# Kernel optimization log

Hardware: AMD Instinct MI355X
Metric: run time of the kernel (lower is better)

Reference implementation:

```python
import jax, jax.numpy as jnp
import numpy as np

B, T, C = 4, 2048, 1024
NH = 16
HS = C // NH


def setup_inputs() -> dict:
    key = jax.random.key(0)
    ks = jax.random.split(key, 11)
    s = 1.0 / np.sqrt(C)
    inp = {
        "query": jax.random.normal(ks[0], (B, T, C), jnp.float32),
        "key": jax.random.normal(ks[1], (B, T, C), jnp.float32),
        "value": jax.random.normal(ks[2], (B, T, C), jnp.float32),
        # causal mask: 1.0 where attention is disallowed (j > i)
        "mask": jnp.triu(jnp.ones((T, T), jnp.float32), k=1)[None, None, :, :],
        "Wq": jax.random.normal(ks[3], (C, C), jnp.float32) * s,
        "bq": jnp.zeros((C,), jnp.float32),
        "Wk": jax.random.normal(ks[4], (C, C), jnp.float32) * s,
        "bk": jnp.zeros((C,), jnp.float32),
        "Wv": jax.random.normal(ks[5], (C, C), jnp.float32) * s,
        "bv": jnp.zeros((C,), jnp.float32),
        "Wo": jax.random.normal(ks[6], (C, C), jnp.float32) * s,
        "bo": jnp.zeros((C,), jnp.float32),
    }
    return inp


def _split_heads(x):  # [B,T,C] -> [B,NH,T,HS]
    Bq, Tq, Cq = x.shape
    return x.reshape(Bq, Tq, NH, Cq // NH).transpose(0, 2, 1, 3)


def reference(query, key, value, mask, Wq, bq, Wk, bk, Wv, bv, Wo, bo):
    q = _split_heads(query @ Wq + bq)   # [B,NH,T,HS]
    k = _split_heads(key @ Wk + bk)
    v = _split_heads(value @ Wv + bv)
    scores = jnp.einsum("bhqd,bhkd->bhqk", q, k) / jnp.sqrt(jnp.asarray(HS, q.dtype))
    scores = scores + mask * (-1e9)
    attn = jax.nn.softmax(scores, axis=-1)
    out = jnp.einsum("bhqk,bhkd->bhqd", attn, v)     # [B,NH,T,HS]
    out = out.transpose(0, 2, 1, 3).reshape(query.shape[0], query.shape[1], -1)
    return out @ Wo + bo
```

## Files before the change

kernel.cpp:

```cpp
#include <hip/hip_runtime.h>
#include <hip/hip_bf16.h>
#include <stdint.h>

#define B_ 4
#define T_ 2048
#define C_ 1024
#define NH_ 16
#define HS_ 64

using bf16 = __hip_bfloat16;
typedef __bf16 bf16x8 __attribute__((ext_vector_type(8)));
typedef float f32x4 __attribute__((ext_vector_type(4)));
typedef short short8 __attribute__((ext_vector_type(8)));

__device__ __forceinline__ f32x4 mfma16(bf16x8 a, bf16x8 b, f32x4 c) {
    return __builtin_amdgcn_mfma_f32_16x16x32_bf16(a, b, c, 0, 0, 0);
}

__device__ __forceinline__ float fexp2(float x) {
    return __builtin_amdgcn_exp2f(x);
}

__device__ __forceinline__ short bf16bits(float f) {
    __bf16 b = (__bf16)f;
    return *reinterpret_cast<short*>(&b);
}

__device__ __forceinline__ void gload16(const void* g, void* l) {
    __builtin_amdgcn_global_load_lds(
        (const __attribute__((address_space(1))) void*)g,
        (__attribute__((address_space(3))) void*)l, 16, 0, 0);
}

__device__ __forceinline__ short8 load8(const bf16* p) { return *(const short8*)p; }
__device__ __forceinline__ short8 load8(const float* p) {
    float4 f0 = *(const float4*)p;
    float4 f1 = *(const float4*)(p + 4);
    short8 r;
    r[0] = bf16bits(f0.x); r[1] = bf16bits(f0.y); r[2] = bf16bits(f0.z); r[3] = bf16bits(f0.w);
    r[4] = bf16bits(f1.x); r[5] = bf16bits(f1.y); r[6] = bf16bits(f1.z); r[7] = bf16bits(f1.w);
    return r;
}

__device__ __forceinline__ void storev(bf16* p, float v) { *p = __float2bfloat16(v); }
__device__ __forceinline__ void storev(float* p, float v) { *p = v; }

__device__ __forceinline__ int swz64(int row, int bytecol) {
    return row * 64 + ((((bytecol >> 4) ^ row) & 3) << 4) + (bytecol & 15);
}

template <typename InT>
__device__ __forceinline__ void transpose_body(
    const InT* __restrict__ in, bf16* __restrict__ out, int R, int C, int zb)
{
    __shared__ short tile[64][80];
    const int t = threadIdx.x;
    const size_t batch = (size_t)zb * R * C;
    const int bx = blockIdx.x * 64;
    const int by = blockIdx.y * 64;
    const int r = t >> 3, c8 = (t & 7) * 8;

    *(short8*)&tile[r][c8]      = load8(in + batch + (size_t)(by + r) * C + bx + c8);
    *(short8*)&tile[r + 32][c8] = load8(in + batch + (size_t)(by + r + 32) * C + bx + c8);
    __syncthreads();
    short8 v0, v1;
    #pragma unroll
    for (int i = 0; i < 8; ++i) {
        v0[i] = tile[c8 + i][r];
        v1[i] = tile[c8 + i][r + 32];
    }
    *(short8*)(out + batch + (size_t)(bx + r) * R + by + c8)      = v0;
    *(short8*)(out + batch + (size_t)(bx + r + 32) * R + by + c8) = v1;
}

__global__ __launch_bounds__(256) void transpose_v_kernel(
    const bf16* __restrict__ in, bf16* __restrict__ out)
{
    transpose_body<bf16>(in, out, T_, HS_, blockIdx.z);
}

__global__ __launch_bounds__(256) void transpose_w4_kernel(
    const float* __restrict__ Wq, const float* __restrict__ Wk,
    const float* __restrict__ Wv, const float* __restrict__ Wo,
    bf16* __restrict__ WqT, bf16* __restrict__ WkT,
    bf16* __restrict__ WvT, bf16* __restrict__ WoT)
{
    const int z = blockIdx.z;
    const float* in = (z == 0) ? Wq : (z == 1) ? Wk : (z == 2) ? Wv : Wo;
    bf16* out      = (z == 0) ? WqT : (z == 1) ? WkT : (z == 2) ? WvT : WoT;
    transpose_body<float>(in, out, 1024, 1024, 0);
}

template <int MODE, typename AT, typename OutT>
__device__ __forceinline__ void gemm_body(
    const AT* __restrict__ A, const bf16* __restrict__ BT,
    const float* __restrict__ bias, OutT* __restrict__ out,
    int M, int N, int K)
{
    constexpr bool A_BF16 = (sizeof(AT) == 2);
    __shared__ __align__(16) short As[128 * 32];
    __shared__ __align__(16) short Bs[128 * 32];
    const int tid = threadIdx.x;
    const int lane = tid & 63;
    const int w = tid >> 6;
    const int wm = w >> 1, wn = w & 1;
    const int lg = lane >> 4, lr = lane & 15;
    const int bm = blockIdx.x * 128;
    const int bn = blockIdx.y * 128;

    const int grow = w * 16 + (lane >> 2);
    const int gch  = (lane & 3) ^ (grow & 3);
    const bf16* gB0 = BT + (size_t)(bn + grow) * K + gch * 8;
    const AT*   gA0 = A  + (size_t)(bm + grow) * K + gch * 8;
    char* lB0 = (char*)Bs + w * 1024;
    char* lA0 = (char*)As + w * 1024;

    const int sr = tid >> 2;
    const int sc = (tid & 3) * 16;
    const AT* gA = A + (size_t)(bm + sr) * K + (tid & 3) * 8;

    f32x4 acc[4][4] = {};

    for (int k0 = 0; k0 < K; k0 += 32) {
        __syncthreads();
        gload16(gB0 + k0, lB0);
        gload16(gB0 + (size_t)64 * K + k0, lB0 + 4096);
        if constexpr (A_BF16) {
            gload16(gA0 + k0, lA0);
            gload16(gA0 + (size_t)64 * K + k0, lA0 + 4096);
        } else {
            short8 a0 = load8(gA + k0);
            short8 a1 = load8(gA + (size_t)64 * K + k0);
            *(short8*)((char*)As + swz64(sr, sc))      = a0;
            *(short8*)((char*)As + swz64(sr + 64, sc)) = a1;
        }
        __syncthreads();
        bf16x8 af[4], bfv[4];
        #pragma unroll
        for (int i = 0; i < 4; ++i) {
            af[i]  = *(const bf16x8*)((char*)As + swz64(wm * 64 + i * 16 + lr, lg * 16));
            bfv[i] = *(const bf16x8*)((char*)Bs + swz64(wn * 64 + i * 16 + lr, lg * 16));
        }
        #pragma unroll
        for (int mi = 0; mi < 4; ++mi)
            #pragma unroll
            for (int nj = 0; nj < 4; ++nj)
                acc[mi][nj] = mfma16(af[mi], bfv[nj], acc[mi][nj]);
    }

    #pragma unroll
    for (int mi = 0; mi < 4; ++mi) {
        #pragma unroll
        for (int nj = 0; nj < 4; ++nj) {
            const int n = bn + wn * 64 + nj * 16 + lr;
            const float bv = bias[n];
            #pragma unroll
            for (int r = 0; r < 4; ++r) {
                const int m = bm + wm * 64 + mi * 16 + lg * 4 + r;
                const float val = acc[mi][nj][r] + bv;
                size_t idx;
                if (MODE == 1) {
                    idx = (size_t)((m >> 11) * NH_ + (n >> 6)) * (T_ * HS_)
                        + (size_t)(m & (T_ - 1)) * HS_ + (n & (HS_ - 1));
                } else {
                    idx = (size_t)m * N + n;
                }
                storev(out + idx, val);
            }
        }
    }
}

__global__ __launch_bounds__(256) void gemm_qkv_kernel(
    const float* __restrict__ Xq, const float* __restrict__ Xk, const float* __restrict__ Xv,
    const bf16* __restrict__ WqT, const bf16* __restrict__ WkT, const bf16* __restrict__ WvT,
    const float* __restrict__ bq, const float* __restrict__ bk, const float* __restrict__ bv,
    bf16* __restrict__ Qh, bf16* __restrict__ Kh, bf16* __restrict__ Vh)
{
    const int z = blockIdx.z;
    const float* A  = (z == 0) ? Xq : (z == 1) ? Xk : Xv;
    const bf16* BT  = (z == 0) ? WqT : (z == 1) ? WkT : WvT;
    const float* bs = (z == 0) ? bq : (z == 1) ? bk : bv;
    bf16* out       = (z == 0) ? Qh : (z == 1) ? Kh : Vh;
    gemm_body<1, float, bf16>(A, BT, bs, out, 8192, 1024, 1024);
}

__global__ __launch_bounds__(256) void gemm_out_kernel(
    const bf16* __restrict__ A, const bf16* __restrict__ BT,
    const float* __restrict__ bias, float* __restrict__ out)
{
    gemm_body<0, bf16, float>(A, BT, bias, out, 8192, 1024, 1024);
}

__global__ __launch_bounds__(512, 4) void attn_kernel(
    const bf16* __restrict__ Qh, const bf16* __restrict__ Kh,
    const bf16* __restrict__ Vt, bf16* __restrict__ Ob)
{
    __shared__ __align__(16) char Ks[2][8192];
    __shared__ __align__(16) char Vs[2][8192];
    __shared__ __align__(16) char Ps[8][2][2048];

    const int tid  = threadIdx.x;
    const int lane = tid & 63;
    const int w    = tid >> 6;
    const int lg = lane >> 4, lr = lane & 15;
    const int bh = blockIdx.x;
    const int bq = blockIdx.y;
    const size_t hb = (size_t)bh * (T_ * HS_);

    const int s_lo = bq * 8 + w;
    const int s_hi = 127 - s_lo;
    const int qbase[2] = { s_lo * 16, s_hi * 16 };
    const int last_t[2] = { s_lo >> 2, s_hi >> 2 };
    const int nt = 32 - 2 * bq;

    const int swzp = (lr & 7) << 4;
    const float SC = 0.125f * 1.44269504088896f;

    const int strow = tid >> 3;
    const int stch  = tid & 7;
    const int stdst = strow * 128 + ((stch ^ (strow & 7)) << 4);
    const bf16* gK = Kh + hb + (size_t)strow * HS_ + stch * 8;
    const bf16* gV = Vt + hb + (size_t)strow * T_  + stch * 8;

    bf16x8 qf[2][2];
    #pragma unroll
    for (int qs = 0; qs < 2; ++qs)
        #pragma unroll
        for (int kfi = 0; kfi < 2; ++kfi)
            qf[qs][kfi] = *(const bf16x8*)(Qh + hb + (size_t)(qbase[qs] + lr) * HS_ + kfi * 32 + lg * 8);

    f32x4 accO[2][4] = {};
    float m_s[2] = {-1e30f, -1e30f};
    float l_s[2] = {0.f, 0.f};
    char* pwq[2] = {&Ps[w][0][0], &Ps[w][1][0]};

    uint4 kst = *(const uint4*)(gK);
    uint4 vst = *(const uint4*)(gV);
    *(uint4*)(&Ks[0][stdst]) = kst;
    *(uint4*)(&Vs[0][stdst]) = vst;
    __syncthreads();

    int c = 0;
    for (int t = 0; t < nt; ++t) {
        if (t + 1 < nt) {
            kst = *(const uint4*)(gK + (size_t)(t + 1) * 64 * HS_);
            vst = *(const uint4*)(gV + (t + 1) * 64);
        }
        const int j0 = t * 64;
        const char* Kc = &Ks[c][0];
        const char* Vc = &Vs[c][0];
        const bool act[2] = { t <= last_t[0], t <= last_t[1] };

        bf16x8 kfr[4][2];
        #pragma unroll
        for (int s = 0; s < 4; ++s)
            #pragma unroll
            for (int kfi = 0; kfi < 2; ++kfi)
                kfr[s][kfi] = *(const bf16x8*)(Kc + (s * 16 + lr) * 128 + (((kfi * 4 + lg) ^ (lr & 7)) << 4));

        #pragma unroll
        for (int qs = 0; qs < 2; ++qs) {
            if (!act[qs]) continue;
            f32x4 st[4];
            #pragma unroll
            for (int s = 0; s < 4; ++s) {
                f32x4 a = {};
                #pragma unroll
                for (int kfi = 0; kfi < 2; ++kfi)
                    a = mfma16(kfr[s][kfi], qf[qs][kfi], a);
                st[s] = a;
            }
            float p[4][4];
            #pragma unroll
            for (int s = 0; s < 4; ++s)
                #pragma unroll
                for (int r = 0; r < 4; ++r)
                    p[s][r] = st[s][r] * SC;
            if (t == last_t[qs]) {
                const int q = qbase[qs] + lr;
                #pragma unroll
                for (int s = 0; s < 4; ++s)
                    #pragma unroll
                    for (int r = 0; r < 4; ++r)
                        if (j0 + s * 16 + 4 * lg + r > q) p[s][r] = -1e30f;
            }
            float mx0 = fmaxf(fmaxf(p[0][0], p[0][1]), fmaxf(p[0][2], p[0][3]));
            float mx1 = fmaxf(fmaxf(p[1][0], p[1][1]), fmaxf(p[1][2], p[1][3]));
            float mx2 = fmaxf(fmaxf(p[2][0], p[2][1]), fmaxf(p[2][2], p[2][3]));
            float mx3 = fmaxf(fmaxf(p[3][0], p[3][1]), fmaxf(p[3][2], p[3][3]));
            float mxin = fmaxf(fmaxf(mx0, mx1), fmaxf(mx2, mx3));
            if (!__all(mxin <= m_s[qs] + 8.0f)) {
                float mx = mxin;
                mx = fmaxf(mx, __shfl_xor(mx, 16));
                mx = fmaxf(mx, __shfl_xor(mx, 32));
                const float mnew = fmaxf(m_s[qs], mx);
                const float sf = fexp2(m_s[qs] - mnew);
                m_s[qs] = mnew;
                l_s[qs] *= sf;
                f32x4 sfv;
                #pragma unroll
                for (int r = 0; r < 4; ++r)
                    sfv[r] = __shfl(sf, 4 * lg + r);
                #pragma unroll
                for (int d = 0; d < 4; ++d)
                    accO[qs][d] *= sfv;
            }
            float rs = 0.f;
            #pragma unroll
            for (int s = 0; s < 4; ++s)
                #pragma unroll
                for (int r = 0; r < 4; ++r) {
                    p[s][r] = fexp2(p[s][r] - m_s[qs]);
                    rs += p[s][r];
                }
            l_s[qs] += rs;
            #pragma unroll
            for (int s = 0; s < 4; ++s) {
                uint2 pk;
                pk.x = (uint16_t)bf16bits(p[s][0]) | ((uint32_t)(uint16_t)bf16bits(p[s][1]) << 16);
                pk.y = (uint16_t)bf16bits(p[s][2]) | ((uint32_t)(uint16_t)bf16bits(p[s][3]) << 16);
                *(uint2*)(pwq[qs] + ((lr * 128 + s * 32 + lg * 8) ^ swzp)) = pk;
            }
        }
        __builtin_amdgcn_wave_barrier();

        bf16x8 vfr[4][2];
        #pragma unroll
        for (int d = 0; d < 4; ++d)
            #pragma unroll
            for (int kfi = 0; kfi < 2; ++kfi)
                vfr[d][kfi] = *(const bf16x8*)(Vc + (d * 16 + lr) * 128 + (((kfi * 4 + lg) ^ (lr & 7)) << 4));

        #pragma unroll
        for (int qs = 0; qs < 2; ++qs) {
            if (!act[qs]) continue;
            bf16x8 aP[2];
            #pragma unroll
            for (int kfi = 0; kfi < 2; ++kfi)
                aP[kfi] = *(const bf16x8*)(pwq[qs] + ((lr * 128 + kfi * 64 + lg * 16) ^ swzp));
            #pragma unroll
            for (int d = 0; d < 4; ++d)
                #pragma unroll
                for (int kfi = 0; kfi < 2; ++kfi)
                    accO[qs][d] = mfma16(aP[kfi], vfr[d][kfi], accO[qs][d]);
        }

        if (t + 1 < nt) {
            *(uint4*)(&Ks[c ^ 1][stdst]) = kst;
            *(uint4*)(&Vs[c ^ 1][stdst]) = vst;
        }
        __syncthreads();
        c ^= 1;
    }

    const int b = bh >> 4, h = bh & 15;
    #pragma unroll
    for (int qs = 0; qs < 2; ++qs) {
        float lsv[4];
        #pragma unroll
        for (int r = 0; r < 4; ++r) {
            float acc = 0.f;
            #pragma unroll
            for (int g = 0; g < 4; ++g)
                acc += __shfl(l_s[qs], 4 * lg + r + 16 * g);
            lsv[r] = acc;
        }
        #pragma unroll
        for (int d = 0; d < 4; ++d)
            #pragma unroll
            for (int r = 0; r < 4; ++r) {
                const int q = qbase[qs] + 4 * lg + r;
                const float o = accO[qs][d][r] / lsv[r];
                Ob[(((size_t)b * T_ + q) * NH_ + h) * HS_ + d * 16 + lr] = __float2bfloat16(o);
            }
    }
}

extern "C" void kernel_launch(void* const* d_in, const int* in_sizes, int n_in,
                              void* d_out, int out_size, void* d_ws, size_t ws_size,
                              hipStream_t stream)
{
    (void)in_sizes; (void)n_in; (void)out_size; (void)ws_size;
    const float* Xq = (const float*)d_in[0];
    const float* Xk = (const float*)d_in[1];
    const float* Xv = (const float*)d_in[2];
    const float* Wq = (const float*)d_in[4];
    const float* bq = (const float*)d_in[5];
    const float* Wk = (const float*)d_in[6];
    const float* bk = (const float*)d_in[7];
    const float* Wv = (const float*)d_in[8];
    const float* bv = (const float*)d_in[9];
    const float* Wo = (const float*)d_in[10];
    const float* bo = (const float*)d_in[11];

    char* ws = (char*)d_ws;
    bf16* WqT = (bf16*)(ws + ((size_t)0  << 20));
    bf16* WkT = (bf16*)(ws + ((size_t)2  << 20));
    bf16* WvT = (bf16*)(ws + ((size_t)4  << 20));
    bf16* WoT = (bf16*)(ws + ((size_t)6  << 20));
    bf16* Qh  = (bf16*)(ws + ((size_t)8  << 20));
    bf16* Kh  = (bf16*)(ws + ((size_t)24 << 20));
    bf16* Vh  = (bf16*)(ws + ((size_t)40 << 20));
    bf16* VtG = (bf16*)(ws + ((size_t)56 << 20));
    bf16* Ob  = (bf16*)(ws + ((size_t)72 << 20));

    dim3 blk(256);
    transpose_w4_kernel<<<dim3(16, 16, 4), blk, 0, stream>>>(
        Wq, Wk, Wv, Wo, WqT, WkT, WvT, WoT);

    gemm_qkv_kernel<<<dim3(64, 8, 3), blk, 0, stream>>>(
        Xq, Xk, Xv, WqT, WkT, WvT, bq, bk, bv, Qh, Kh, Vh);

    transpose_v_kernel<<<dim3(1, 32, B_ * NH_), blk, 0, stream>>>(Vh, VtG);

    attn_kernel<<<dim3(64, 8), dim3(512), 0, stream>>>(Qh, Kh, VtG, Ob);

    gemm_out_kernel<<<dim3(64, 8), blk, 0, stream>>>(Ob, WoT, bo, (float*)d_out);
}
```

Baseline: 210.1 us.

## Write V transposed from QKV GEMM and double GEMM K-tile to 64

The QKV GEMM epilogue now writes V directly in the per-head transposed layout the attention kernel reads, which removes the separate V transpose kernel, one launch and a round trip of V through memory. Separately, the GEMM K step grows from 32 to 64, using wider LDS tiles with an 8-chunk XOR swizzle, so there are half as many barrier-separated load/compute iterations. The transposed V store is strided along T, so those writes are less coalesced. The larger shared-memory tiles may also reduce occupancy.

```diff
diff --git a/kernel.cpp b/kernel.cpp
--- a/kernel.cpp
+++ b/kernel.cpp
@@ -44,10 +44,6 @@
 
 __device__ __forceinline__ void storev(bf16* p, float v) { *p = __float2bfloat16(v); }
 __device__ __forceinline__ void storev(float* p, float v) { *p = v; }
-
-__device__ __forceinline__ int swz64(int row, int bytecol) {
-    return row * 64 + ((((bytecol >> 4) ^ row) & 3) << 4) + (bytecol & 15);
-}
 
 template <typename InT>
 __device__ __forceinline__ void transpose_body(
@@ -73,12 +69,6 @@
     *(short8*)(out + batch + (size_t)(bx + r + 32) * R + by + c8) = v1;
 }
 
-__global__ __launch_bounds__(256) void transpose_v_kernel(
-    const bf16* __restrict__ in, bf16* __restrict__ out)
-{
-    transpose_body<bf16>(in, out, T_, HS_, blockIdx.z);
-}
-
 __global__ __launch_bounds__(256) void transpose_w4_kernel(
     const float* __restrict__ Wq, const float* __restrict__ Wk,
     const float* __restrict__ Wv, const float* __restrict__ Wo,
@@ -91,15 +81,15 @@
     transpose_body<float>(in, out, 1024, 1024, 0);
 }
 
-template <int MODE, typename AT, typename OutT>
+template <typename AT, typename OutT>
 __device__ __forceinline__ void gemm_body(
     const AT* __restrict__ A, const bf16* __restrict__ BT,
     const float* __restrict__ bias, OutT* __restrict__ out,
-    int M, int N, int K)
+    int M, int N, int K, int mode)
 {
     constexpr bool A_BF16 = (sizeof(AT) == 2);
-    __shared__ __align__(16) short As[128 * 32];
-    __shared__ __align__(16) short Bs[128 * 32];
+    __shared__ __align__(16) short As[128 * 64];
+    __shared__ __align__(16) short Bs[128 * 64];
     const int tid = threadIdx.x;
     const int lane = tid & 63;
     const int w = tid >> 6;
@@ -108,44 +98,51 @@
     const int bm = blockIdx.x * 128;
     const int bn = blockIdx.y * 128;
 
-    const int grow = w * 16 + (lane >> 2);
-    const int gch  = (lane & 3) ^ (grow & 3);
-    const bf16* gB0 = BT + (size_t)(bn + grow) * K + gch * 8;
-    const AT*   gA0 = A  + (size_t)(bm + grow) * K + gch * 8;
-    char* lB0 = (char*)Bs + w * 1024;
-    char* lA0 = (char*)As + w * 1024;
-
-    const int sr = tid >> 2;
-    const int sc = (tid & 3) * 16;
-    const AT* gA = A + (size_t)(bm + sr) * K + (tid & 3) * 8;
+    const int rowi = lane >> 3;
+    const int gch  = (lane & 7) ^ rowi;
+    const bf16* gB0 = BT + (size_t)(bn + w * 32 + rowi) * K + gch * 8;
+    const AT*   gA0 = A  + (size_t)(bm + w * 32 + rowi) * K + gch * 8;
+    char* lB0 = (char*)Bs + w * 4096;
+    char* lA0 = (char*)As + w * 4096;
+
+    const int arow = tid >> 3;
+    const int achk = tid & 7;
+    const AT* gA = A + (size_t)(bm + arow) * K + achk * 8;
+    const int awsw = (achk ^ (arow & 7)) << 4;
 
     f32x4 acc[4][4] = {};
-
-    for (int k0 = 0; k0 < K; k0 += 32) {
+    const int rsw = lr & 7;
+
+    for (int k0 = 0; k0 < K; k0 += 64) {
         __syncthreads();
-        gload16(gB0 + k0, lB0);
-        gload16(gB0 + (size_t)64 * K + k0, lB0 + 4096);
-        if constexpr (A_BF16) {
-            gload16(gA0 + k0, lA0);
-            gload16(gA0 + (size_t)64 * K + k0, lA0 + 4096);
-        } else {
-            short8 a0 = load8(gA + k0);
-            short8 a1 = load8(gA + (size_t)64 * K + k0);
-            *(short8*)((char*)As + swz64(sr, sc))      = a0;
-            *(short8*)((char*)As + swz64(sr + 64, sc)) = a1;
+        #pragma unroll
+        for (int i = 0; i < 4; ++i) {
+            gload16(gB0 + (size_t)i * 8 * K + k0, lB0 + i * 1024);
+            if constexpr (A_BF16)
+                gload16(gA0 + (size_t)i * 8 * K + k0, lA0 + i * 1024);
+        }
+        if constexpr (!A_BF16) {
+            #pragma unroll
+            for (int j = 0; j < 4; ++j) {
+                short8 a0 = load8(gA + (size_t)j * 32 * K + k0);
+                *(short8*)((char*)As + (arow + j * 32) * 128 + awsw) = a0;
+            }
         }
         __syncthreads();
-        bf16x8 af[4], bfv[4];
-        #pragma unroll
-        for (int i = 0; i < 4; ++i) {
-            af[i]  = *(const bf16x8*)((char*)As + swz64(wm * 64 + i * 16 + lr, lg * 16));
-            bfv[i] = *(const bf16x8*)((char*)Bs + swz64(wn * 64 + i * 16 + lr, lg * 16));
-        }
-        #pragma unroll
-        for (int mi = 0; mi < 4; ++mi)
-            #pragma unroll
-            for (int nj = 0; nj < 4; ++nj)
-                acc[mi][nj] = mfma16(af[mi], bfv[nj], acc[mi][nj]);
+        #pragma unroll
+        for (int kfi = 0; kfi < 2; ++kfi) {
+            bf16x8 af[4], bfv[4];
+            #pragma unroll
+            for (int i = 0; i < 4; ++i) {
+                af[i]  = *(const bf16x8*)((char*)As + (wm * 64 + i * 16 + lr) * 128 + (((kfi * 4 + lg) ^ rsw) << 4));
+                bfv[i] = *(const bf16x8*)((char*)Bs + (wn * 64 + i * 16 + lr) * 128 + (((kfi * 4 + lg) ^ rsw) << 4));
+            }
+            #pragma unroll
+            for (int mi = 0; mi < 4; ++mi)
+                #pragma unroll
+                for (int nj = 0; nj < 4; ++nj)
+                    acc[mi][nj] = mfma16(af[mi], bfv[nj], acc[mi][nj]);
+        }
     }
 
     #pragma unroll
@@ -159,9 +156,12 @@
                 const int m = bm + wm * 64 + mi * 16 + lg * 4 + r;
                 const float val = acc[mi][nj][r] + bv;
                 size_t idx;
-                if (MODE == 1) {
+                if (mode == 1) {
                     idx = (size_t)((m >> 11) * NH_ + (n >> 6)) * (T_ * HS_)
                         + (size_t)(m & (T_ - 1)) * HS_ + (n & (HS_ - 1));
+                } else if (mode == 2) {
+                    idx = (size_t)((m >> 11) * NH_ + (n >> 6)) * (T_ * HS_)
+                        + (size_t)(n & (HS_ - 1)) * T_ + (m & (T_ - 1));
                 } else {
                     idx = (size_t)m * N + n;
                 }
@@ -175,21 +175,21 @@
     const float* __restrict__ Xq, const float* __restrict__ Xk, const float* __restrict__ Xv,
     const bf16* __restrict__ WqT, const bf16* __restrict__ WkT, const bf16* __restrict__ WvT,
     const float* __restrict__ bq, const float* __restrict__ bk, const float* __restrict__ bv,
-    bf16* __restrict__ Qh, bf16* __restrict__ Kh, bf16* __restrict__ Vh)
+    bf16* __restrict__ Qh, bf16* __restrict__ Kh, bf16* __restrict__ VtG)
 {
     const int z = blockIdx.z;
     const float* A  = (z == 0) ? Xq : (z == 1) ? Xk : Xv;
     const bf16* BT  = (z == 0) ? WqT : (z == 1) ? WkT : WvT;
     const float* bs = (z == 0) ? bq : (z == 1) ? bk : bv;
-    bf16* out       = (z == 0) ? Qh : (z == 1) ? Kh : Vh;
-    gemm_body<1, float, bf16>(A, BT, bs, out, 8192, 1024, 1024);
+    bf16* out       = (z == 0) ? Qh : (z == 1) ? Kh : VtG;
+    gemm_body<float, bf16>(A, BT, bs, out, 8192, 1024, 1024, (z == 2) ? 2 : 1);
 }
 
 __global__ __launch_bounds__(256) void gemm_out_kernel(
     const bf16* __restrict__ A, const bf16* __restrict__ BT,
     const float* __restrict__ bias, float* __restrict__ out)
 {
-    gemm_body<0, bf16, float>(A, BT, bias, out, 8192, 1024, 1024);
+    gemm_body<bf16, float>(A, BT, bias, out, 8192, 1024, 1024, 0);
 }
 
 __global__ __launch_bounds__(512, 4) void attn_kernel(
@@ -401,18 +401,15 @@
     bf16* WoT = (bf16*)(ws + ((size_t)6  << 20));
     bf16* Qh  = (bf16*)(ws + ((size_t)8  << 20));
     bf16* Kh  = (bf16*)(ws + ((size_t)24 << 20));
-    bf16* Vh  = (bf16*)(ws + ((size_t)40 << 20));
-    bf16* VtG = (bf16*)(ws + ((size_t)56 << 20));
-    bf16* Ob  = (bf16*)(ws + ((size_t)72 << 20));
+    bf16* VtG = (bf16*)(ws + ((size_t)40 << 20));
+    bf16* Ob  = (bf16*)(ws + ((size_t)56 << 20));
 
     dim3 blk(256);
     transpose_w4_kernel<<<dim3(16, 16, 4), blk, 0, stream>>>(
         Wq, Wk, Wv, Wo, WqT, WkT, WvT, WoT);
 
     gemm_qkv_kernel<<<dim3(64, 8, 3), blk, 0, stream>>>(
-        Xq, Xk, Xv, WqT, WkT, WvT, bq, bk, bv, Qh, Kh, Vh);
-
-    transpose_v_kernel<<<dim3(1, 32, B_ * NH_), blk, 0, stream>>>(Vh, VtG);
+        Xq, Xk, Xv, WqT, WkT, WvT, bq, bk, bv, Qh, Kh, VtG);
 
     attn_kernel<<<dim3(64, 8), dim3(512), 0, stream>>>(Qh, Kh, VtG, Ob);
 
```

Result: slower. 215.8 us (+2.7%).

## Fuse V transpose into QKV GEMM epilogue and widen GEMM tiles to 128x256

Applied to the files above, without the earlier changes.

The QKV GEMM now writes V straight into the head-transposed layout the attention kernel reads, so the separate V transpose kernel and its round trip through global memory are gone. Both GEMMs also move from 256-thread 128x128 tiles to 512-thread 128x256 tiles (8 waves in a 2x4 layout), which raises reuse of each loaded A tile. The tradeoffs: the transposed V store is strided along T and coalesces worse, the output mode is now a runtime branch instead of a template parameter, and the grid has half as many blocks.

```diff
diff --git a/kernel.cpp b/kernel.cpp
--- a/kernel.cpp
+++ b/kernel.cpp
@@ -73,12 +73,6 @@
     *(short8*)(out + batch + (size_t)(bx + r + 32) * R + by + c8) = v1;
 }
 
-__global__ __launch_bounds__(256) void transpose_v_kernel(
-    const bf16* __restrict__ in, bf16* __restrict__ out)
-{
-    transpose_body<bf16>(in, out, T_, HS_, blockIdx.z);
-}
-
 __global__ __launch_bounds__(256) void transpose_w4_kernel(
     const float* __restrict__ Wq, const float* __restrict__ Wk,
     const float* __restrict__ Wv, const float* __restrict__ Wo,
@@ -91,28 +85,31 @@
     transpose_body<float>(in, out, 1024, 1024, 0);
 }
 
-template <int MODE, typename AT, typename OutT>
+template <typename AT, typename OutT>
 __device__ __forceinline__ void gemm_body(
     const AT* __restrict__ A, const bf16* __restrict__ BT,
     const float* __restrict__ bias, OutT* __restrict__ out,
-    int M, int N, int K)
+    int M, int N, int K, int mode)
 {
     constexpr bool A_BF16 = (sizeof(AT) == 2);
     __shared__ __align__(16) short As[128 * 32];
-    __shared__ __align__(16) short Bs[128 * 32];
+    __shared__ __align__(16) short Bs[256 * 32];
     const int tid = threadIdx.x;
     const int lane = tid & 63;
     const int w = tid >> 6;
-    const int wm = w >> 1, wn = w & 1;
+    const int wm = w >> 2, wn = w & 3;
     const int lg = lane >> 4, lr = lane & 15;
     const int bm = blockIdx.x * 128;
-    const int bn = blockIdx.y * 128;
-
-    const int grow = w * 16 + (lane >> 2);
-    const int gch  = (lane & 3) ^ (grow & 3);
-    const bf16* gB0 = BT + (size_t)(bn + grow) * K + gch * 8;
-    const AT*   gA0 = A  + (size_t)(bm + grow) * K + gch * 8;
-    char* lB0 = (char*)Bs + w * 1024;
+    const int bn = blockIdx.y * 256;
+
+    const int brow = w * 32 + (lane >> 2);
+    const int gchb = (lane & 3) ^ (brow & 3);
+    const bf16* gB0 = BT + (size_t)(bn + brow) * K + gchb * 8;
+    char* lB0 = (char*)Bs + w * 2048;
+
+    const int arow = w * 16 + (lane >> 2);
+    const int gcha = (lane & 3) ^ (arow & 3);
+    const AT* gA0 = A + (size_t)(bm + arow) * K + gcha * 8;
     char* lA0 = (char*)As + w * 1024;
 
     const int sr = tid >> 2;
@@ -124,15 +121,12 @@
     for (int k0 = 0; k0 < K; k0 += 32) {
         __syncthreads();
         gload16(gB0 + k0, lB0);
-        gload16(gB0 + (size_t)64 * K + k0, lB0 + 4096);
+        gload16(gB0 + (size_t)16 * K + k0, lB0 + 1024);
         if constexpr (A_BF16) {
             gload16(gA0 + k0, lA0);
-            gload16(gA0 + (size_t)64 * K + k0, lA0 + 4096);
         } else {
             short8 a0 = load8(gA + k0);
-            short8 a1 = load8(gA + (size_t)64 * K + k0);
-            *(short8*)((char*)As + swz64(sr, sc))      = a0;
-            *(short8*)((char*)As + swz64(sr + 64, sc)) = a1;
+            *(short8*)((char*)As + swz64(sr, sc)) = a0;
         }
         __syncthreads();
         bf16x8 af[4], bfv[4];
@@ -159,9 +153,12 @@
                 const int m = bm + wm * 64 + mi * 16 + lg * 4 + r;
                 const float val = acc[mi][nj][r] + bv;
                 size_t idx;
-                if (MODE == 1) {
+                if (mode == 1) {
                     idx = (size_t)((m >> 11) * NH_ + (n >> 6)) * (T_ * HS_)
                         + (size_t)(m & (T_ - 1)) * HS_ + (n & (HS_ - 1));
+                } else if (mode == 2) {
+                    idx = (size_t)((m >> 11) * NH_ + (n >> 6)) * (T_ * HS_)
+                        + (size_t)(n & (HS_ - 1)) * T_ + (m & (T_ - 1));
                 } else {
                     idx = (size_t)m * N + n;
                 }
@@ -171,25 +168,25 @@
     }
 }
 
-__global__ __launch_bounds__(256) void gemm_qkv_kernel(
+__global__ __launch_bounds__(512, 2) void gemm_qkv_kernel(
     const float* __restrict__ Xq, const float* __restrict__ Xk, const float* __restrict__ Xv,
     const bf16* __restrict__ WqT, const bf16* __restrict__ WkT, const bf16* __restrict__ WvT,
     const float* __restrict__ bq, const float* __restrict__ bk, const float* __restrict__ bv,
-    bf16* __restrict__ Qh, bf16* __restrict__ Kh, bf16* __restrict__ Vh)
+    bf16* __restrict__ Qh, bf16* __restrict__ Kh, bf16* __restrict__ VtG)
 {
     const int z = blockIdx.z;
     const float* A  = (z == 0) ? Xq : (z == 1) ? Xk : Xv;
     const bf16* BT  = (z == 0) ? WqT : (z == 1) ? WkT : WvT;
     const float* bs = (z == 0) ? bq : (z == 1) ? bk : bv;
-    bf16* out       = (z == 0) ? Qh : (z == 1) ? Kh : Vh;
-    gemm_body<1, float, bf16>(A, BT, bs, out, 8192, 1024, 1024);
-}
-
-__global__ __launch_bounds__(256) void gemm_out_kernel(
+    bf16* out       = (z == 0) ? Qh : (z == 1) ? Kh : VtG;
+    gemm_body<float, bf16>(A, BT, bs, out, 8192, 1024, 1024, (z == 2) ? 2 : 1);
+}
+
+__global__ __launch_bounds__(512, 2) void gemm_out_kernel(
     const bf16* __restrict__ A, const bf16* __restrict__ BT,
     const float* __restrict__ bias, float* __restrict__ out)
 {
-    gemm_body<0, bf16, float>(A, BT, bias, out, 8192, 1024, 1024);
+    gemm_body<bf16, float>(A, BT, bias, out, 8192, 1024, 1024, 0);
 }
 
 __global__ __launch_bounds__(512, 4) void attn_kernel(
@@ -401,20 +398,16 @@
     bf16* WoT = (bf16*)(ws + ((size_t)6  << 20));
     bf16* Qh  = (bf16*)(ws + ((size_t)8  << 20));
     bf16* Kh  = (bf16*)(ws + ((size_t)24 << 20));
-    bf16* Vh  = (bf16*)(ws + ((size_t)40 << 20));
-    bf16* VtG = (bf16*)(ws + ((size_t)56 << 20));
-    bf16* Ob  = (bf16*)(ws + ((size_t)72 << 20));
-
-    dim3 blk(256);
-    transpose_w4_kernel<<<dim3(16, 16, 4), blk, 0, stream>>>(
+    bf16* VtG = (bf16*)(ws + ((size_t)40 << 20));
+    bf16* Ob  = (bf16*)(ws + ((size_t)56 << 20));
+
+    transpose_w4_kernel<<<dim3(16, 16, 4), dim3(256), 0, stream>>>(
         Wq, Wk, Wv, Wo, WqT, WkT, WvT, WoT);
 
-    gemm_qkv_kernel<<<dim3(64, 8, 3), blk, 0, stream>>>(
-        Xq, Xk, Xv, WqT, WkT, WvT, bq, bk, bv, Qh, Kh, Vh);
-
-    transpose_v_kernel<<<dim3(1, 32, B_ * NH_), blk, 0, stream>>>(Vh, VtG);
+    gemm_qkv_kernel<<<dim3(64, 4, 3), dim3(512), 0, stream>>>(
+        Xq, Xk, Xv, WqT, WkT, WvT, bq, bk, bv, Qh, Kh, VtG);
 
     attn_kernel<<<dim3(64, 8), dim3(512), 0, stream>>>(Qh, Kh, VtG, Ob);
 
-    gemm_out_kernel<<<dim3(64, 8), blk, 0, stream>>>(Ob, WoT, bo, (float*)d_out);
-}
+    gemm_out_kernel<<<dim3(64, 4), dim3(512), 0, stream>>>(Ob, WoT, bo, (float*)d_out);
+}
```

New measurement: 239.8 us. +14.1%, slower.

## Pre-convert activations to bf16 and write V transposed from GEMM epilogue

Applied to the files above, without the earlier changes.

Adds a conversion kernel that turns fp32 query/key/value inputs into bf16 buffers, so the projection GEMMs can load A tiles with direct global-to-LDS async loads instead of converting through registers. The V projection now writes its output directly in the transposed per-head layout the attention kernel needs, which removes the separate V transpose kernel. The trade-off is an extra full read and write pass over the activations for conversion, plus strided, uncoalesced stores in the V epilogue. The QKV GEMM is also split into two launches with workspace buffers reused between them.

```diff
diff --git a/kernel.cpp b/kernel.cpp
--- a/kernel.cpp
+++ b/kernel.cpp
@@ -47,6 +47,16 @@
 
 __device__ __forceinline__ int swz64(int row, int bytecol) {
     return row * 64 + ((((bytecol >> 4) ^ row) & 3) << 4) + (bytecol & 15);
+}
+
+__global__ __launch_bounds__(256) void convert_x_kernel(
+    const float* __restrict__ s0, const float* __restrict__ s1,
+    bf16* __restrict__ d0, bf16* __restrict__ d1)
+{
+    const float* s = blockIdx.y ? s1 : s0;
+    bf16* d       = blockIdx.y ? d1 : d0;
+    const size_t i = ((size_t)blockIdx.x * 256 + threadIdx.x) * 8;
+    *(short8*)(d + i) = load8(s + i);
 }
 
 template <typename InT>
@@ -73,12 +83,6 @@
     *(short8*)(out + batch + (size_t)(bx + r + 32) * R + by + c8) = v1;
 }
 
-__global__ __launch_bounds__(256) void transpose_v_kernel(
-    const bf16* __restrict__ in, bf16* __restrict__ out)
-{
-    transpose_body<bf16>(in, out, T_, HS_, blockIdx.z);
-}
-
 __global__ __launch_bounds__(256) void transpose_w4_kernel(
     const float* __restrict__ Wq, const float* __restrict__ Wk,
     const float* __restrict__ Wv, const float* __restrict__ Wo,
@@ -91,13 +95,12 @@
     transpose_body<float>(in, out, 1024, 1024, 0);
 }
 
-template <int MODE, typename AT, typename OutT>
+template <typename OutT>
 __device__ __forceinline__ void gemm_body(
-    const AT* __restrict__ A, const bf16* __restrict__ BT,
+    const bf16* __restrict__ A, const bf16* __restrict__ BT,
     const float* __restrict__ bias, OutT* __restrict__ out,
-    int M, int N, int K)
-{
-    constexpr bool A_BF16 = (sizeof(AT) == 2);
+    int M, int N, int K, int mode)
+{
     __shared__ __align__(16) short As[128 * 32];
     __shared__ __align__(16) short Bs[128 * 32];
     const int tid = threadIdx.x;
@@ -111,13 +114,9 @@
     const int grow = w * 16 + (lane >> 2);
     const int gch  = (lane & 3) ^ (grow & 3);
     const bf16* gB0 = BT + (size_t)(bn + grow) * K + gch * 8;
-    const AT*   gA0 = A  + (size_t)(bm + grow) * K + gch * 8;
+    const bf16* gA0 = A  + (size_t)(bm + grow) * K + gch * 8;
     char* lB0 = (char*)Bs + w * 1024;
     char* lA0 = (char*)As + w * 1024;
-
-    const int sr = tid >> 2;
-    const int sc = (tid & 3) * 16;
-    const AT* gA = A + (size_t)(bm + sr) * K + (tid & 3) * 8;
 
     f32x4 acc[4][4] = {};
 
@@ -125,15 +124,8 @@
         __syncthreads();
         gload16(gB0 + k0, lB0);
         gload16(gB0 + (size_t)64 * K + k0, lB0 + 4096);
-        if constexpr (A_BF16) {
-            gload16(gA0 + k0, lA0);
-            gload16(gA0 + (size_t)64 * K + k0, lA0 + 4096);
-        } else {
-            short8 a0 = load8(gA + k0);
-            short8 a1 = load8(gA + (size_t)64 * K + k0);
-            *(short8*)((char*)As + swz64(sr, sc))      = a0;
-            *(short8*)((char*)As + swz64(sr + 64, sc)) = a1;
-        }
+        gload16(gA0 + k0, lA0);
+        gload16(gA0 + (size_t)64 * K + k0, lA0 + 4096);
         __syncthreads();
         bf16x8 af[4], bfv[4];
         #pragma unroll
@@ -159,9 +151,12 @@
                 const int m = bm + wm * 64 + mi * 16 + lg * 4 + r;
                 const float val = acc[mi][nj][r] + bv;
                 size_t idx;
-                if (MODE == 1) {
+                if (mode == 1) {
                     idx = (size_t)((m >> 11) * NH_ + (n >> 6)) * (T_ * HS_)
                         + (size_t)(m & (T_ - 1)) * HS_ + (n & (HS_ - 1));
+                } else if (mode == 2) {
+                    idx = (size_t)((m >> 11) * NH_ + (n >> 6)) * (T_ * HS_)
+                        + (size_t)(n & (HS_ - 1)) * T_ + (m & (T_ - 1));
                 } else {
                     idx = (size_t)m * N + n;
                 }
@@ -171,25 +166,29 @@
     }
 }
 
-__global__ __launch_bounds__(256) void gemm_qkv_kernel(
-    const float* __restrict__ Xq, const float* __restrict__ Xk, const float* __restrict__ Xv,
-    const bf16* __restrict__ WqT, const bf16* __restrict__ WkT, const bf16* __restrict__ WvT,
-    const float* __restrict__ bq, const float* __restrict__ bk, const float* __restrict__ bv,
-    bf16* __restrict__ Qh, bf16* __restrict__ Kh, bf16* __restrict__ Vh)
+__global__ __launch_bounds__(256) void gemm_qk_kernel(
+    const bf16* __restrict__ XbA, const bf16* __restrict__ XbB,
+    const bf16* __restrict__ WqT, const bf16* __restrict__ WkT,
+    const float* __restrict__ bq, const float* __restrict__ bk,
+    bf16* __restrict__ Qh, bf16* __restrict__ Kh)
 {
     const int z = blockIdx.z;
-    const float* A  = (z == 0) ? Xq : (z == 1) ? Xk : Xv;
-    const bf16* BT  = (z == 0) ? WqT : (z == 1) ? WkT : WvT;
-    const float* bs = (z == 0) ? bq : (z == 1) ? bk : bv;
-    bf16* out       = (z == 0) ? Qh : (z == 1) ? Kh : Vh;
-    gemm_body<1, float, bf16>(A, BT, bs, out, 8192, 1024, 1024);
+    gemm_body<bf16>(z ? XbB : XbA, z ? WkT : WqT, z ? bk : bq,
+                    z ? Kh : Qh, 8192, 1024, 1024, 1);
+}
+
+__global__ __launch_bounds__(256) void gemm_v_kernel(
+    const bf16* __restrict__ Xb, const bf16* __restrict__ WvT,
+    const float* __restrict__ bv, bf16* __restrict__ VtG)
+{
+    gemm_body<bf16>(Xb, WvT, bv, VtG, 8192, 1024, 1024, 2);
 }
 
 __global__ __launch_bounds__(256) void gemm_out_kernel(
     const bf16* __restrict__ A, const bf16* __restrict__ BT,
     const float* __restrict__ bias, float* __restrict__ out)
 {
-    gemm_body<0, bf16, float>(A, BT, bias, out, 8192, 1024, 1024);
+    gemm_body<float>(A, BT, bias, out, 8192, 1024, 1024, 0);
 }
 
 __global__ __launch_bounds__(512, 4) void attn_kernel(
@@ -399,20 +398,25 @@
     bf16* WkT = (bf16*)(ws + ((size_t)2  << 20));
     bf16* WvT = (bf16*)(ws + ((size_t)4  << 20));
     bf16* WoT = (bf16*)(ws + ((size_t)6  << 20));
-    bf16* Qh  = (bf16*)(ws + ((size_t)8  << 20));
-    bf16* Kh  = (bf16*)(ws + ((size_t)24 << 20));
-    bf16* Vh  = (bf16*)(ws + ((size_t)40 << 20));
-    bf16* VtG = (bf16*)(ws + ((size_t)56 << 20));
-    bf16* Ob  = (bf16*)(ws + ((size_t)72 << 20));
+    bf16* XbA = (bf16*)(ws + ((size_t)8  << 20));
+    bf16* XbB = (bf16*)(ws + ((size_t)24 << 20));
+    bf16* Qh  = (bf16*)(ws + ((size_t)40 << 20));
+    bf16* Kh  = (bf16*)(ws + ((size_t)56 << 20));
+    bf16* VtG = (bf16*)(ws + ((size_t)72 << 20));
+    bf16* Ob  = XbB;
 
     dim3 blk(256);
     transpose_w4_kernel<<<dim3(16, 16, 4), blk, 0, stream>>>(
         Wq, Wk, Wv, Wo, WqT, WkT, WvT, WoT);
 
-    gemm_qkv_kernel<<<dim3(64, 8, 3), blk, 0, stream>>>(
-        Xq, Xk, Xv, WqT, WkT, WvT, bq, bk, bv, Qh, Kh, Vh);
-
-    transpose_v_kernel<<<dim3(1, 32, B_ * NH_), blk, 0, stream>>>(Vh, VtG);
+    convert_x_kernel<<<dim3(4096, 2), blk, 0, stream>>>(Xq, Xk, XbA, XbB);
+
+    gemm_qk_kernel<<<dim3(64, 8, 2), blk, 0, stream>>>(
+        XbA, XbB, WqT, WkT, bq, bk, Qh, Kh);
+
+    convert_x_kernel<<<dim3(4096, 1), blk, 0, stream>>>(Xv, Xv, XbA, XbA);
+
+    gemm_v_kernel<<<dim3(64, 8), blk, 0, stream>>>(XbA, WvT, bv, VtG);
 
     attn_kernel<<<dim3(64, 8), dim3(512), 0, stream>>>(Qh, Kh, VtG, Ob);
 
```

Result: slower. 218.1 us (+3.8%).
